# Kernel optimization log

Measured on AMD Instinct MI355X. Metric: run time of the kernel, lower is better.

The kernel has to match this reference:

```python
import jax, jax.numpy as jnp
import numpy as np

T, H, E, I, K = 8192, 2048, 32, 1024, 2


def setup_inputs() -> dict:
    key = jax.random.key(0)
    ks = jax.random.split(key, 6)
    s = 1.0 / np.sqrt(H)
    return {
        "hidden_states": jax.random.normal(ks[0], (T, H), dtype=jnp.float32),
        "router_logits": jax.random.normal(ks[1], (T, E), dtype=jnp.float32),
        "per_expert_scale": jax.random.uniform(ks[2], (E,), dtype=jnp.float32, minval=0.5, maxval=1.5),
        "w_gate": jax.random.normal(ks[3], (E, H, I), dtype=jnp.float32) * s,
        "w_up": jax.random.normal(ks[4], (E, H, I), dtype=jnp.float32) * s,
        "w_down": jax.random.normal(ks[5], (E, I, H), dtype=jnp.float32) * (1.0 / np.sqrt(I)),
        "top_k": K,
    }


def reference(hidden_states, router_logits, per_expert_scale, w_gate, w_up, w_down, top_k):
    num_tokens, hidden_dim = hidden_states.shape
    num_experts = w_gate.shape[0]
    # Gemma4 routing: top-k over raw logits, softmax over the k logits
    # (== full softmax renormalized over top-k), scaled per expert.
    topk_logits, topk_ids = jax.lax.top_k(router_logits, top_k)  # [T,K]
    topk_weights = jax.nn.softmax(topk_logits, axis=-1) * per_expert_scale[topk_ids]
    # Dense combine matrix [T,E]: weight for expert e if selected, else 0.
    cw = jnp.zeros((num_tokens, num_experts), hidden_states.dtype)
    cw = cw.at[jnp.arange(num_tokens)[:, None], topk_ids].add(
        topk_weights.astype(hidden_states.dtype))
    # Gated GELU MLP per expert, weighted accumulate (scan keeps memory small).
    def body(acc, ws):
        wg, wu, wd, c = ws  # c: [T] combine weight for this expert
        h = jax.nn.gelu(hidden_states @ wg, approximate=False) * (hidden_states @ wu)
        return acc + c[:, None] * (h @ wd), None
    acc0 = jnp.zeros_like(hidden_states)
    out, _ = jax.lax.scan(body, acc0, (w_gate, w_up, w_down, cw.T))
    return out
```

## Files before the change

kernel.cpp:

```cpp
#include <hip/hip_runtime.h>

#define T_TOK 8192
#define HDIM  2048
#define NEXP  32
#define IDIM  1024

#define BM 128
#define BN 128
#define BK 64
#define CAP (T_TOK*2 + NEXP*BM)
#define MAX_RT (CAP/BM)

typedef __attribute__((ext_vector_type(8))) short bh8;
typedef __attribute__((ext_vector_type(4))) float f4;

__device__ __forceinline__ unsigned short f2bf(float f) {
    unsigned u = __builtin_bit_cast(unsigned, f);
    u += 0x7FFFu + ((u >> 16) & 1u);
    return (unsigned short)(u >> 16);
}

__device__ __forceinline__ int swz(int row, int kb) {
    return row * 128 + (kb ^ ((row & 7) << 4));
}


__device__ __forceinline__ void top2(const float* __restrict__ l,
                                     int& b1, float& v1, int& b2, float& v2) {
    v1 = -1e30f; b1 = 0;
#pragma unroll
    for (int e = 0; e < NEXP; ++e) { float v = l[e]; if (v > v1) { v1 = v; b1 = e; } }
    v2 = -1e30f; b2 = 0;
#pragma unroll
    for (int e = 0; e < NEXP; ++e) { if (e == b1) continue; float v = l[e]; if (v > v2) { v2 = v; b2 = e; } }
}

__global__ void route_count_kernel(const float* __restrict__ logits, int* __restrict__ counts) {
    int t = blockIdx.x * blockDim.x + threadIdx.x;
    if (t >= T_TOK) return;
    int b1, b2; float v1, v2;
    top2(logits + (size_t)t * NEXP, b1, v1, b2, v2);
    atomicAdd(&counts[b1], 1);
    atomicAdd(&counts[b2], 1);
}

__global__ void offsets_kernel(const int* __restrict__ counts, int* __restrict__ offs) {
    if (threadIdx.x == 0) {
        int o = 0;
        for (int e = 0; e < NEXP; ++e) { offs[e] = o; o += (counts[e] + BM - 1) & ~(BM - 1); }
        offs[NEXP] = o;
    }
}

__global__ void route_scatter_kernel(const float* __restrict__ logits,
                                     const float* __restrict__ scale,
                                     const int* __restrict__ offs,
                                     int* __restrict__ cursor,
                                     int* __restrict__ row_tok,
                                     float* __restrict__ row_w) {
    int t = blockIdx.x * blockDim.x + threadIdx.x;
    if (t >= T_TOK) return;
    int b1, b2; float v1, v2;
    top2(logits + (size_t)t * NEXP, b1, v1, b2, v2);
    float e2 = expf(v2 - v1);
    float inv = 1.0f / (1.0f + e2);
    float w1 = scale[b1] * inv;
    float w2 = scale[b2] * e2 * inv;
    int p1 = offs[b1] + atomicAdd(&cursor[b1], 1);
    row_tok[p1] = t; row_w[p1] = w1;
    int p2 = offs[b2] + atomicAdd(&cursor[b2], 1);
    row_tok[p2] = t; row_w[p2] = w2;
}


__device__ __forceinline__ void stage_w(char* dst, const float* __restrict__ src,
                                        long stride, int wn, int wk) {
    float t[32];
#pragma unroll
    for (int kk = 0; kk < 32; ++kk) t[kk] = src[kk * stride];
#pragma unroll
    for (int j = 0; j < 4; ++j) {
        bh8 p;
#pragma unroll
        for (int i = 0; i < 8; ++i) p[i] = (short)f2bf(t[j * 8 + i]);
        *(bh8*)(dst + swz(wn, wk * 64 + j * 16)) = p;
    }
}


__launch_bounds__(256, 2)
__global__ void gemm1_kernel(const float* __restrict__ hs,
                             const float* __restrict__ wg,
                             const float* __restrict__ wu,
                             const int* __restrict__ offs,
                             const int* __restrict__ row_tok,
                             unsigned short* __restrict__ act) {
    __shared__ char lds[48 * 1024];
    char* Xb = lds;
    char* Gb = lds + 16384;
    char* Ub = lds + 32768;

    int rt = blockIdx.x >> 3;
    int nt = blockIdx.x & 7;
    int total = offs[NEXP];
    if (rt * BM >= total) return;
    int e = 0;
    while (offs[e + 1] <= rt * BM) e++;

    int tid = threadIdx.x;
    int lane = tid & 63;
    int wv = tid >> 6;
    int m0 = wv * 32;

    int sr = tid >> 1;
    int sh = tid & 1;
    int tok = row_tok[rt * BM + sr];
    const float* xsrc = hs + (size_t)(tok < 0 ? 0 : tok) * HDIM + sh * 32;

    int wn = tid & 127;
    int wk = tid >> 7;
    const float* wgs = wg + (size_t)e * HDIM * IDIM + (size_t)(wk * 32) * IDIM + nt * BN + wn;
    const float* wus = wu + (size_t)e * HDIM * IDIM + (size_t)(wk * 32) * IDIM + nt * BN + wn;

    f4 accG[2][8], accU[2][8];
#pragma unroll
    for (int m = 0; m < 2; ++m)
#pragma unroll
        for (int n = 0; n < 8; ++n) { accG[m][n] = (f4)0.0f; accU[m][n] = (f4)0.0f; }

    for (int kt = 0; kt < HDIM / BK; ++kt) {
        {
            float4 v[8];
#pragma unroll
            for (int j = 0; j < 8; ++j) v[j] = make_float4(0.f, 0.f, 0.f, 0.f);
            if (tok >= 0) {
                const float4* p = (const float4*)(xsrc + kt * BK);
#pragma unroll
                for (int j = 0; j < 8; ++j) v[j] = p[j];
            }
#pragma unroll
            for (int j = 0; j < 4; ++j) {
                float4 a = v[2 * j], b = v[2 * j + 1];
                bh8 p;
                p[0] = (short)f2bf(a.x); p[1] = (short)f2bf(a.y);
                p[2] = (short)f2bf(a.z); p[3] = (short)f2bf(a.w);
                p[4] = (short)f2bf(b.x); p[5] = (short)f2bf(b.y);
                p[6] = (short)f2bf(b.z); p[7] = (short)f2bf(b.w);
                *(bh8*)(Xb + swz(sr, sh * 64 + j * 16)) = p;
            }
        }
        stage_w(Gb, wgs + (size_t)kt * BK * IDIM, IDIM, wn, wk);
        stage_w(Ub, wus + (size_t)kt * BK * IDIM, IDIM, wn, wk);
        __syncthreads();

#pragma unroll
        for (int ks = 0; ks < 2; ++ks) {
            int kb = ks * 64 + ((lane >> 4) << 4);
            bh8 a0 = *(const bh8*)(Xb + swz(m0 + (lane & 15), kb));
            bh8 a1 = *(const bh8*)(Xb + swz(m0 + 16 + (lane & 15), kb));
#pragma unroll
            for (int n = 0; n < 8; ++n) {
                int nr = n * 16 + (lane & 15);
                bh8 bg = *(const bh8*)(Gb + swz(nr, kb));
                bh8 bu = *(const bh8*)(Ub + swz(nr, kb));
                accG[0][n] = __builtin_amdgcn_mfma_f32_16x16x32_bf16(a0, bg, accG[0][n], 0, 0, 0);
                accG[1][n] = __builtin_amdgcn_mfma_f32_16x16x32_bf16(a1, bg, accG[1][n], 0, 0, 0);
                accU[0][n] = __builtin_amdgcn_mfma_f32_16x16x32_bf16(a0, bu, accU[0][n], 0, 0, 0);
                accU[1][n] = __builtin_amdgcn_mfma_f32_16x16x32_bf16(a1, bu, accU[1][n], 0, 0, 0);
            }
        }
        __syncthreads();
    }

    int col0 = nt * BN + (lane & 15);
#pragma unroll
    for (int m = 0; m < 2; ++m) {
        int rbase = rt * BM + m0 + m * 16 + ((lane >> 4) << 2);
#pragma unroll
        for (int n = 0; n < 8; ++n) {
#pragma unroll
            for (int i = 0; i < 4; ++i) {
                float g = accG[m][n][i], u = accU[m][n][i];
                float gl = 0.5f * g * (1.0f + erff(g * 0.70710678118654752f));
                act[(size_t)(rbase + i) * IDIM + col0 + n * 16] = f2bf(gl * u);
            }
        }
    }
}


__launch_bounds__(256, 2)
__global__ void gemm2_kernel(const unsigned short* __restrict__ act,
                             const float* __restrict__ wd,
                             const int* __restrict__ offs,
                             const int* __restrict__ row_tok,
                             const float* __restrict__ row_w,
                             float* __restrict__ out) {
    __shared__ char lds[32 * 1024];
    char* Xb = lds;
    char* Db = lds + 16384;

    int rt = blockIdx.x >> 4;
    int nt = blockIdx.x & 15;
    int total = offs[NEXP];
    if (rt * BM >= total) return;
    int e = 0;
    while (offs[e + 1] <= rt * BM) e++;

    int tid = threadIdx.x;
    int lane = tid & 63;
    int wv = tid >> 6;
    int m0 = wv * 32;

    int sr = tid >> 1;
    int sh = tid & 1;
    const unsigned short* asrc = act + (size_t)(rt * BM + sr) * IDIM + sh * 32;

    int wn = tid & 127;
    int wk = tid >> 7;
    const float* wds = wd + (size_t)e * IDIM * HDIM + (size_t)(wk * 32) * HDIM + nt * BN + wn;

    f4 acc[2][8];
#pragma unroll
    for (int m = 0; m < 2; ++m)
#pragma unroll
        for (int n = 0; n < 8; ++n) acc[m][n] = (f4)0.0f;

    for (int kt = 0; kt < IDIM / BK; ++kt) {
        {
            const bh8* p = (const bh8*)(asrc + kt * BK);
#pragma unroll
            for (int j = 0; j < 4; ++j)
                *(bh8*)(Xb + swz(sr, sh * 64 + j * 16)) = p[j];
        }
        stage_w(Db, wds + (size_t)kt * BK * HDIM, HDIM, wn, wk);
        __syncthreads();

#pragma unroll
        for (int ks = 0; ks < 2; ++ks) {
            int kb = ks * 64 + ((lane >> 4) << 4);
            bh8 a0 = *(const bh8*)(Xb + swz(m0 + (lane & 15), kb));
            bh8 a1 = *(const bh8*)(Xb + swz(m0 + 16 + (lane & 15), kb));
#pragma unroll
            for (int n = 0; n < 8; ++n) {
                int nr = n * 16 + (lane & 15);
                bh8 b = *(const bh8*)(Db + swz(nr, kb));
                acc[0][n] = __builtin_amdgcn_mfma_f32_16x16x32_bf16(a0, b, acc[0][n], 0, 0, 0);
                acc[1][n] = __builtin_amdgcn_mfma_f32_16x16x32_bf16(a1, b, acc[1][n], 0, 0, 0);
            }
        }
        __syncthreads();
    }

    int col0 = nt * BN + (lane & 15);
#pragma unroll
    for (int m = 0; m < 2; ++m) {
        int rbase = rt * BM + m0 + m * 16 + ((lane >> 4) << 2);
#pragma unroll
        for (int i = 0; i < 4; ++i) {
            int r = rbase + i;
            int tok = row_tok[r];
            if (tok < 0) continue;
            float w = row_w[r];
            float* op = out + (size_t)tok * HDIM + col0;
#pragma unroll
            for (int n = 0; n < 8; ++n)
                atomicAdd(op + n * 16, acc[m][n][i] * w);
        }
    }
}


extern "C" void kernel_launch(void* const* d_in, const int* in_sizes, int n_in,
                              void* d_out, int out_size, void* d_ws, size_t ws_size,
                              hipStream_t stream) {
    const float* hs     = (const float*)d_in[0];
    const float* logits = (const float*)d_in[1];
    const float* scale  = (const float*)d_in[2];
    const float* wg     = (const float*)d_in[3];
    const float* wu     = (const float*)d_in[4];
    const float* wd     = (const float*)d_in[5];
    float* out = (float*)d_out;

    char* ws = (char*)d_ws;
    int*   counts  = (int*)ws;
    int*   cursor  = counts + 32;
    int*   offs    = cursor + 32;
    int*   row_tok = (int*)(ws + 512);
    float* row_w   = (float*)(ws + 512 + (size_t)CAP * 4);
    unsigned short* act = (unsigned short*)(ws + 512 + (size_t)CAP * 8);

    hipMemsetAsync(counts, 0, 512, stream);
    hipMemsetAsync(row_tok, 0xFF, (size_t)CAP * 4, stream);
    hipMemsetAsync(out, 0, (size_t)out_size * sizeof(float), stream);

    route_count_kernel<<<T_TOK / 256, 256, 0, stream>>>(logits, counts);
    offsets_kernel<<<1, 64, 0, stream>>>(counts, offs);
    route_scatter_kernel<<<T_TOK / 256, 256, 0, stream>>>(logits, scale, offs, cursor, row_tok, row_w);
    gemm1_kernel<<<MAX_RT * 8, 256, 0, stream>>>(hs, wg, wu, offs, row_tok, act);
    gemm2_kernel<<<MAX_RT * 16, 256, 0, stream>>>(act, wd, offs, row_tok, row_w, out);
}
```

Measured before the change: 805.3 us.

## Pre-convert activations and weights to transposed bf16, use direct-to-LDS loads in GEMMs

New measurement: 745.9 us. 1.08x faster.

```diff
diff --git a/kernel.cpp b/kernel.cpp
--- a/kernel.cpp
+++ b/kernel.cpp
@@ -22,6 +22,13 @@
 
 __device__ __forceinline__ int swz(int row, int kb) {
     return row * 128 + (kb ^ ((row & 7) << 4));
+}
+
+__device__ __forceinline__ void gload16(const void* g, void* l) {
+    __builtin_amdgcn_global_load_lds(
+        (const __attribute__((address_space(1))) unsigned int*)g,
+        (__attribute__((address_space(3))) unsigned int*)l,
+        16, 0, 0);
 }
 
 
@@ -73,6 +80,244 @@
 }
 
 
+__global__ void cvt_hs_kernel(const float* __restrict__ in, unsigned short* __restrict__ out) {
+    size_t i = ((size_t)blockIdx.x * 256 + threadIdx.x) * 8;
+    float4 a = *(const float4*)(in + i);
+    float4 b = *(const float4*)(in + i + 4);
+    bh8 v;
+    v[0] = (short)f2bf(a.x); v[1] = (short)f2bf(a.y);
+    v[2] = (short)f2bf(a.z); v[3] = (short)f2bf(a.w);
+    v[4] = (short)f2bf(b.x); v[5] = (short)f2bf(b.y);
+    v[6] = (short)f2bf(b.z); v[7] = (short)f2bf(b.w);
+    *(bh8*)(out + i) = v;
+}
+
+__global__ void transpose_cvt_kernel(const float* __restrict__ in,
+                                     unsigned short* __restrict__ out,
+                                     int K, int N, int tilesN) {
+    int bid = blockIdx.x;
+    int e = bid >> 9;
+    int tile = bid & 511;
+    int k0 = (tile / tilesN) * 64;
+    int n0 = (tile % tilesN) * 64;
+    const float* src = in + (size_t)e * K * N;
+    unsigned short* dst = out + (size_t)e * K * N;
+    int tid = threadIdx.x, l = tid & 63, w = tid >> 6;
+    int n = n0 + w * 16 + (l >> 2);
+#pragma unroll
+    for (int p = 0; p < 2; ++p) {
+        int kc = k0 + p * 32 + (l & 3) * 8;
+        const float* s = src + (size_t)kc * N + n;
+        bh8 v;
+#pragma unroll
+        for (int j = 0; j < 8; ++j) v[j] = (short)f2bf(s[(size_t)j * N]);
+        *(bh8*)(dst + (size_t)n * K + kc) = v;
+    }
+}
+
+__launch_bounds__(256, 2)
+__global__ void gemm1n_kernel(const unsigned short* __restrict__ hsb,
+                              const unsigned short* __restrict__ wgT,
+                              const unsigned short* __restrict__ wuT,
+                              const int* __restrict__ offs,
+                              const int* __restrict__ row_tok,
+                              unsigned short* __restrict__ act) {
+    __shared__ char lds[49152];
+    char* Xb = lds;
+    char* Gb = lds + 16384;
+    char* Ub = lds + 32768;
+
+    int rt = blockIdx.x >> 3;
+    int nt = blockIdx.x & 7;
+    int total = offs[NEXP];
+    if (rt * BM >= total) return;
+    int e = 0;
+    while (offs[e + 1] <= rt * BM) e++;
+
+    int tid = threadIdx.x, l = tid & 63, wv = tid >> 6;
+    int wm = wv >> 1, wn = wv & 1;
+
+    unsigned srcChunk = ((l & 7) * 16) ^ ((l >> 3) << 4);
+
+    unsigned xoff[4], goff[4], uoff[4];
+#pragma unroll
+    for (int i = 0; i < 4; ++i) {
+        int r = i * 32 + wv * 8 + (l >> 3);
+        int tok = row_tok[rt * BM + r];
+        if (tok < 0) tok = 0;
+        xoff[i] = (unsigned)tok * (HDIM * 2) + srcChunk;
+        unsigned wrow = (unsigned)e * IDIM + nt * BN + r;
+        goff[i] = wrow * (HDIM * 2) + srcChunk;
+        uoff[i] = goff[i];
+    }
+
+    f4 accG[4][4], accU[4][4];
+#pragma unroll
+    for (int mi = 0; mi < 4; ++mi)
+#pragma unroll
+        for (int ni = 0; ni < 4; ++ni) { accG[mi][ni] = (f4)0.0f; accU[mi][ni] = (f4)0.0f; }
+
+    const char* hsc = (const char*)hsb;
+    const char* wgc = (const char*)wgT;
+    const char* wuc = (const char*)wuT;
+
+    for (int kt = 0; kt < HDIM / BK; ++kt) {
+        unsigned kby = kt * 128;
+#pragma unroll
+        for (int i = 0; i < 4; ++i) {
+            char* dX = Xb + i * 4096 + wv * 1024;
+            gload16(hsc + (size_t)xoff[i] + kby, dX);
+        }
+#pragma unroll
+        for (int i = 0; i < 4; ++i) {
+            char* dG = Gb + i * 4096 + wv * 1024;
+            gload16(wgc + (size_t)goff[i] + kby, dG);
+        }
+#pragma unroll
+        for (int i = 0; i < 4; ++i) {
+            char* dU = Ub + i * 4096 + wv * 1024;
+            gload16(wuc + (size_t)uoff[i] + kby, dU);
+        }
+        __syncthreads();
+
+#pragma unroll
+        for (int ks = 0; ks < 2; ++ks) {
+            int kb = ks * 64 + ((l >> 4) << 4);
+            bh8 a[4], g[4], u[4];
+#pragma unroll
+            for (int mi = 0; mi < 4; ++mi)
+                a[mi] = *(const bh8*)(Xb + swz(wm * 64 + mi * 16 + (l & 15), kb));
+#pragma unroll
+            for (int ni = 0; ni < 4; ++ni) {
+                int nr = wn * 64 + ni * 16 + (l & 15);
+                g[ni] = *(const bh8*)(Gb + swz(nr, kb));
+                u[ni] = *(const bh8*)(Ub + swz(nr, kb));
+            }
+#pragma unroll
+            for (int mi = 0; mi < 4; ++mi)
+#pragma unroll
+                for (int ni = 0; ni < 4; ++ni) {
+                    accG[mi][ni] = __builtin_amdgcn_mfma_f32_16x16x32_bf16(a[mi], g[ni], accG[mi][ni], 0, 0, 0);
+                    accU[mi][ni] = __builtin_amdgcn_mfma_f32_16x16x32_bf16(a[mi], u[ni], accU[mi][ni], 0, 0, 0);
+                }
+        }
+        __syncthreads();
+    }
+
+    char* actc = (char*)act;
+#pragma unroll
+    for (int mi = 0; mi < 4; ++mi) {
+#pragma unroll
+        for (int i = 0; i < 4; ++i) {
+            int r = rt * BM + wm * 64 + mi * 16 + ((l >> 4) << 2) + i;
+            size_t rowbase = (size_t)r * (IDIM * 2);
+            int rs = (r & 7) << 4;
+#pragma unroll
+            for (int ni = 0; ni < 4; ++ni) {
+                int col = nt * BN + wn * 64 + ni * 16 + (l & 15);
+                float gv = accG[mi][ni][i], uv = accU[mi][ni][i];
+                float gl = 0.5f * gv * (1.0f + erff(gv * 0.70710678118654752f));
+                *(unsigned short*)(actc + rowbase + ((col * 2) ^ rs)) = f2bf(gl * uv);
+            }
+        }
+    }
+}
+
+__launch_bounds__(256, 2)
+__global__ void gemm2n_kernel(const unsigned short* __restrict__ act,
+                              const unsigned short* __restrict__ wdT,
+                              const int* __restrict__ offs,
+                              const int* __restrict__ row_tok,
+                              const float* __restrict__ row_w,
+                              float* __restrict__ out) {
+    __shared__ char lds[49152];
+    char* Xb = lds;
+    char* Db = lds + 16384;
+
+    int rt = blockIdx.x >> 3;
+    int nt = blockIdx.x & 7;
+    int total = offs[NEXP];
+    if (rt * BM >= total) return;
+    int e = 0;
+    while (offs[e + 1] <= rt * BM) e++;
+
+    int tid = threadIdx.x, l = tid & 63, wv = tid >> 6;
+    int wm = wv >> 1, wn = wv & 1;
+
+    unsigned srcChunk = ((l & 7) * 16) ^ ((l >> 3) << 4);
+
+    unsigned aoff[4];
+#pragma unroll
+    for (int i = 0; i < 4; ++i) {
+        int r = i * 32 + wv * 8 + (l >> 3);
+        aoff[i] = (unsigned)(rt * BM + r) * (IDIM * 2) + (l & 7) * 16;
+    }
+    unsigned doff[8];
+#pragma unroll
+    for (int i = 0; i < 8; ++i) {
+        int r = i * 32 + wv * 8 + (l >> 3);
+        doff[i] = ((unsigned)e * HDIM + nt * 256 + r) * (IDIM * 2) + srcChunk;
+    }
+
+    f4 acc[4][8];
+#pragma unroll
+    for (int mi = 0; mi < 4; ++mi)
+#pragma unroll
+        for (int ni = 0; ni < 8; ++ni) acc[mi][ni] = (f4)0.0f;
+
+    const char* actc = (const char*)act;
+    const char* wdc = (const char*)wdT;
+
+    for (int kt = 0; kt < IDIM / BK; ++kt) {
+        unsigned kby = kt * 128;
+#pragma unroll
+        for (int i = 0; i < 4; ++i) {
+            char* dX = Xb + i * 4096 + wv * 1024;
+            gload16(actc + (size_t)aoff[i] + kby, dX);
+        }
+#pragma unroll
+        for (int i = 0; i < 8; ++i) {
+            char* dD = Db + i * 4096 + wv * 1024;
+            gload16(wdc + (size_t)doff[i] + kby, dD);
+        }
+        __syncthreads();
+
+#pragma unroll
+        for (int ks = 0; ks < 2; ++ks) {
+            int kb = ks * 64 + ((l >> 4) << 4);
+            bh8 a[4], b[8];
+#pragma unroll
+            for (int mi = 0; mi < 4; ++mi)
+                a[mi] = *(const bh8*)(Xb + swz(wm * 64 + mi * 16 + (l & 15), kb));
+#pragma unroll
+            for (int ni = 0; ni < 8; ++ni)
+                b[ni] = *(const bh8*)(Db + swz(wn * 128 + ni * 16 + (l & 15), kb));
+#pragma unroll
+            for (int mi = 0; mi < 4; ++mi)
+#pragma unroll
+                for (int ni = 0; ni < 8; ++ni)
+                    acc[mi][ni] = __builtin_amdgcn_mfma_f32_16x16x32_bf16(a[mi], b[ni], acc[mi][ni], 0, 0, 0);
+        }
+        __syncthreads();
+    }
+
+#pragma unroll
+    for (int mi = 0; mi < 4; ++mi) {
+#pragma unroll
+        for (int i = 0; i < 4; ++i) {
+            int r = rt * BM + wm * 64 + mi * 16 + ((l >> 4) << 2) + i;
+            int tok = row_tok[r];
+            if (tok < 0) continue;
+            float w = row_w[r];
+            float* op = out + (size_t)tok * HDIM + nt * 256 + wn * 128 + (l & 15);
+#pragma unroll
+            for (int ni = 0; ni < 8; ++ni)
+                atomicAdd(op + ni * 16, acc[mi][ni][i] * w);
+        }
+    }
+}
+
+
 __device__ __forceinline__ void stage_w(char* dst, const float* __restrict__ src,
                                         long stride, int wn, int wk) {
     float t[32];
@@ -86,7 +331,6 @@
         *(bh8*)(dst + swz(wn, wk * 64 + j * 16)) = p;
     }
 }
-
 
 __launch_bounds__(256, 2)
 __global__ void gemm1_kernel(const float* __restrict__ hs,
@@ -188,7 +432,6 @@
     }
 }
 
-
 __launch_bounds__(256, 2)
 __global__ void gemm2_kernel(const unsigned short* __restrict__ act,
                              const float* __restrict__ wd,
@@ -290,6 +533,12 @@
     float* row_w   = (float*)(ws + 512 + (size_t)CAP * 4);
     unsigned short* act = (unsigned short*)(ws + 512 + (size_t)CAP * 8);
 
+    size_t actB  = (size_t)CAP * IDIM * 2;
+    size_t hsB   = (size_t)T_TOK * HDIM * 2;
+    size_t wTB   = (size_t)NEXP * IDIM * HDIM * 2;
+    size_t baseA = 512 + (size_t)CAP * 8;
+    size_t needA = baseA + actB + hsB + 2 * wTB;
+
     hipMemsetAsync(counts, 0, 512, stream);
     hipMemsetAsync(row_tok, 0xFF, (size_t)CAP * 4, stream);
     hipMemsetAsync(out, 0, (size_t)out_size * sizeof(float), stream);
@@ -297,6 +546,21 @@
     route_count_kernel<<<T_TOK / 256, 256, 0, stream>>>(logits, counts);
     offsets_kernel<<<1, 64, 0, stream>>>(counts, offs);
     route_scatter_kernel<<<T_TOK / 256, 256, 0, stream>>>(logits, scale, offs, cursor, row_tok, row_w);
-    gemm1_kernel<<<MAX_RT * 8, 256, 0, stream>>>(hs, wg, wu, offs, row_tok, act);
-    gemm2_kernel<<<MAX_RT * 16, 256, 0, stream>>>(act, wd, offs, row_tok, row_w, out);
-}
+
+    if (ws_size >= needA) {
+        unsigned short* hsb = (unsigned short*)(ws + baseA + actB);
+        unsigned short* wgT = (unsigned short*)(ws + baseA + actB + hsB);
+        unsigned short* wuT = (unsigned short*)(ws + baseA + actB + hsB + wTB);
+        unsigned short* wdT = wgT;
+
+        cvt_hs_kernel<<<(T_TOK * HDIM) / (256 * 8), 256, 0, stream>>>(hs, hsb);
+        transpose_cvt_kernel<<<NEXP * 512, 256, 0, stream>>>(wg, wgT, HDIM, IDIM, 16);
+        transpose_cvt_kernel<<<NEXP * 512, 256, 0, stream>>>(wu, wuT, HDIM, IDIM, 16);
+        gemm1n_kernel<<<MAX_RT * 8, 256, 0, stream>>>(hsb, wgT, wuT, offs, row_tok, act);
+        transpose_cvt_kernel<<<NEXP * 512, 256, 0, stream>>>(wd, wdT, IDIM, HDIM, 32);
+        gemm2n_kernel<<<MAX_RT * 8, 256, 0, stream>>>(act, wdT, offs, row_tok, row_w, out);
+    } else {
+        gemm1_kernel<<<MAX_RT * 8, 256, 0, stream>>>(hs, wg, wu, offs, row_tok, act);
+        gemm2_kernel<<<MAX_RT * 16, 256, 0, stream>>>(act, wd, offs, row_tok, row_w, out);
+    }
+}
```

## Pre-convert activations to bf16 and software-pipeline both expert GEMMs with async LDS loads

Applied to the files above, without the earlier changes.

Result: slower. 2.120 ms (+163.2%).

```diff
diff --git a/kernel.cpp b/kernel.cpp
--- a/kernel.cpp
+++ b/kernel.cpp
@@ -22,6 +22,16 @@
 
 __device__ __forceinline__ int swz(int row, int kb) {
     return row * 128 + (kb ^ ((row & 7) << 4));
+}
+__device__ __forceinline__ int swzW(int row, int kb) {
+    return row * 128 + (kb ^ (((row >> 2) & 7) << 4));
+}
+
+__device__ __forceinline__ void gload16(const void* g, void* l) {
+    __builtin_amdgcn_global_load_lds(
+        (const __attribute__((address_space(1))) unsigned int*)g,
+        (__attribute__((address_space(3))) unsigned int*)l,
+        16, 0, 0);
 }
 
 
@@ -72,33 +82,30 @@
     row_tok[p2] = t; row_w[p2] = w2;
 }
 
-
-__device__ __forceinline__ void stage_w(char* dst, const float* __restrict__ src,
-                                        long stride, int wn, int wk) {
-    float t[32];
-#pragma unroll
-    for (int kk = 0; kk < 32; ++kk) t[kk] = src[kk * stride];
-#pragma unroll
-    for (int j = 0; j < 4; ++j) {
-        bh8 p;
-#pragma unroll
-        for (int i = 0; i < 8; ++i) p[i] = (short)f2bf(t[j * 8 + i]);
-        *(bh8*)(dst + swz(wn, wk * 64 + j * 16)) = p;
-    }
-}
-
+__global__ void cvt_hs_kernel(const float* __restrict__ in, unsigned short* __restrict__ out) {
+    size_t i = ((size_t)blockIdx.x * 256 + threadIdx.x) * 8;
+    float4 a = *(const float4*)(in + i);
+    float4 b = *(const float4*)(in + i + 4);
+    bh8 v;
+    v[0] = (short)f2bf(a.x); v[1] = (short)f2bf(a.y);
+    v[2] = (short)f2bf(a.z); v[3] = (short)f2bf(a.w);
+    v[4] = (short)f2bf(b.x); v[5] = (short)f2bf(b.y);
+    v[6] = (short)f2bf(b.z); v[7] = (short)f2bf(b.w);
+    *(bh8*)(out + i) = v;
+}
 
 __launch_bounds__(256, 2)
-__global__ void gemm1_kernel(const float* __restrict__ hs,
-                             const float* __restrict__ wg,
-                             const float* __restrict__ wu,
-                             const int* __restrict__ offs,
-                             const int* __restrict__ row_tok,
-                             unsigned short* __restrict__ act) {
-    __shared__ char lds[48 * 1024];
-    char* Xb = lds;
-    char* Gb = lds + 16384;
-    char* Ub = lds + 32768;
+__global__ void gemm1f_kernel(const unsigned short* __restrict__ hsb,
+                              const float* __restrict__ wg,
+                              const float* __restrict__ wu,
+                              const int* __restrict__ offs,
+                              const int* __restrict__ row_tok,
+                              unsigned short* __restrict__ act) {
+    __shared__ char lds[65536];
+    char* Xb0 = lds;
+    char* Xb1 = lds + 16384;
+    char* Gb  = lds + 32768;
+    char* Ub  = lds + 49152;
 
     int rt = blockIdx.x >> 3;
     int nt = blockIdx.x & 7;
@@ -107,98 +114,134 @@
     int e = 0;
     while (offs[e + 1] <= rt * BM) e++;
 
-    int tid = threadIdx.x;
-    int lane = tid & 63;
-    int wv = tid >> 6;
-    int m0 = wv * 32;
-
-    int sr = tid >> 1;
-    int sh = tid & 1;
-    int tok = row_tok[rt * BM + sr];
-    const float* xsrc = hs + (size_t)(tok < 0 ? 0 : tok) * HDIM + sh * 32;
-
-    int wn = tid & 127;
-    int wk = tid >> 7;
-    const float* wgs = wg + (size_t)e * HDIM * IDIM + (size_t)(wk * 32) * IDIM + nt * BN + wn;
-    const float* wus = wu + (size_t)e * HDIM * IDIM + (size_t)(wk * 32) * IDIM + nt * BN + wn;
-
-    f4 accG[2][8], accU[2][8];
-#pragma unroll
-    for (int m = 0; m < 2; ++m)
-#pragma unroll
-        for (int n = 0; n < 8; ++n) { accG[m][n] = (f4)0.0f; accU[m][n] = (f4)0.0f; }
+    int tid = threadIdx.x, l = tid & 63, wv = tid >> 6;
+    int wm = wv >> 1, wn = wv & 1;
+
+    unsigned srcChunk = ((l & 7) * 16) ^ ((l >> 3) << 4);
+    unsigned xoff[4];
+#pragma unroll
+    for (int i = 0; i < 4; ++i) {
+        int r = i * 32 + wv * 8 + (l >> 3);
+        int tok = row_tok[rt * BM + r];
+        if (tok < 0) tok = 0;
+        xoff[i] = (unsigned)tok * (HDIM * 2) + srcChunk;
+    }
+    const char* hsc = (const char*)hsb;
+
+    int g32 = tid & 31, kc8 = tid >> 5;
+    const float* wgp = wg + (size_t)e * HDIM * IDIM + (size_t)kc8 * 8 * IDIM + nt * BN + g32 * 4;
+    const float* wup = wu + (size_t)e * HDIM * IDIM + (size_t)kc8 * 8 * IDIM + nt * BN + g32 * 4;
+    float4 wGr[8], wUr[8];
+
+    f4 accG[4][4], accU[4][4];
+#pragma unroll
+    for (int mi = 0; mi < 4; ++mi)
+#pragma unroll
+        for (int ni = 0; ni < 4; ++ni) { accG[mi][ni] = (f4)0.0f; accU[mi][ni] = (f4)0.0f; }
+
+#define LOADW1(KT) {                                                        \
+    size_t kb_ = (size_t)(KT) * 64;                                         \
+    _Pragma("unroll")                                                       \
+    for (int j = 0; j < 8; ++j) {                                           \
+        wGr[j] = *(const float4*)(wgp + (kb_ + j) * IDIM);                  \
+        wUr[j] = *(const float4*)(wup + (kb_ + j) * IDIM);                  \
+    } }
+
+#define WRITEW1() {                                                         \
+    _Pragma("unroll")                                                       \
+    for (int c = 0; c < 4; ++c) {                                           \
+        int n_ = g32 * 4 + c;                                               \
+        int wb_ = n_ * 128 + ((kc8 * 16) ^ ((g32 & 7) << 4));               \
+        bh8 pg, pu;                                                         \
+        _Pragma("unroll")                                                   \
+        for (int j = 0; j < 8; ++j) {                                       \
+            float gg = (c == 0) ? wGr[j].x : (c == 1) ? wGr[j].y : (c == 2) ? wGr[j].z : wGr[j].w; \
+            float uu = (c == 0) ? wUr[j].x : (c == 1) ? wUr[j].y : (c == 2) ? wUr[j].z : wUr[j].w; \
+            pg[j] = (short)f2bf(gg);                                        \
+            pu[j] = (short)f2bf(uu);                                        \
+        }                                                                   \
+        *(bh8*)(Gb + wb_) = pg;                                             \
+        *(bh8*)(Ub + wb_) = pu;                                             \
+    } }
+
+#define LOADX1(KT, XB) {                                                    \
+    unsigned kby_ = (unsigned)(KT) * 128;                                   \
+    _Pragma("unroll")                                                       \
+    for (int i = 0; i < 4; ++i)                                             \
+        gload16(hsc + (size_t)xoff[i] + kby_, (XB) + i * 4096 + wv * 1024); \
+    }
+
+    LOADW1(0);
+    LOADX1(0, Xb0);
+    WRITEW1();
+    __syncthreads();
 
     for (int kt = 0; kt < HDIM / BK; ++kt) {
-        {
-            float4 v[8];
-#pragma unroll
-            for (int j = 0; j < 8; ++j) v[j] = make_float4(0.f, 0.f, 0.f, 0.f);
-            if (tok >= 0) {
-                const float4* p = (const float4*)(xsrc + kt * BK);
-#pragma unroll
-                for (int j = 0; j < 8; ++j) v[j] = p[j];
+        char* cur = (kt & 1) ? Xb1 : Xb0;
+        char* nxt = (kt & 1) ? Xb0 : Xb1;
+        if (kt < HDIM / BK - 1) {
+            LOADW1(kt + 1);
+            LOADX1(kt + 1, nxt);
+        }
+#pragma unroll
+        for (int ks = 0; ks < 2; ++ks) {
+            int kb = ks * 64 + ((l >> 4) << 4);
+            bh8 a[4], g[4], u[4];
+#pragma unroll
+            for (int mi = 0; mi < 4; ++mi)
+                a[mi] = *(const bh8*)(cur + swz(wm * 64 + mi * 16 + (l & 15), kb));
+#pragma unroll
+            for (int ni = 0; ni < 4; ++ni) {
+                int nr = wn * 64 + ni * 16 + (l & 15);
+                g[ni] = *(const bh8*)(Gb + swzW(nr, kb));
+                u[ni] = *(const bh8*)(Ub + swzW(nr, kb));
             }
 #pragma unroll
-            for (int j = 0; j < 4; ++j) {
-                float4 a = v[2 * j], b = v[2 * j + 1];
-                bh8 p;
-                p[0] = (short)f2bf(a.x); p[1] = (short)f2bf(a.y);
-                p[2] = (short)f2bf(a.z); p[3] = (short)f2bf(a.w);
-                p[4] = (short)f2bf(b.x); p[5] = (short)f2bf(b.y);
-                p[6] = (short)f2bf(b.z); p[7] = (short)f2bf(b.w);
-                *(bh8*)(Xb + swz(sr, sh * 64 + j * 16)) = p;
+            for (int mi = 0; mi < 4; ++mi)
+#pragma unroll
+                for (int ni = 0; ni < 4; ++ni) {
+                    accG[mi][ni] = __builtin_amdgcn_mfma_f32_16x16x32_bf16(a[mi], g[ni], accG[mi][ni], 0, 0, 0);
+                    accU[mi][ni] = __builtin_amdgcn_mfma_f32_16x16x32_bf16(a[mi], u[ni], accU[mi][ni], 0, 0, 0);
+                }
+        }
+        __syncthreads();
+        if (kt < HDIM / BK - 1) WRITEW1();
+        __syncthreads();
+    }
+
+    char* actc = (char*)act;
+#pragma unroll
+    for (int mi = 0; mi < 4; ++mi) {
+#pragma unroll
+        for (int i = 0; i < 4; ++i) {
+            int r = rt * BM + wm * 64 + mi * 16 + ((l >> 4) << 2) + i;
+            size_t rowbase = (size_t)r * (IDIM * 2);
+            int rs = (r & 7) << 4;
+#pragma unroll
+            for (int ni = 0; ni < 4; ++ni) {
+                int col = nt * BN + wn * 64 + ni * 16 + (l & 15);
+                float gv = accG[mi][ni][i], uv = accU[mi][ni][i];
+                float gl = 0.5f * gv * (1.0f + erff(gv * 0.70710678118654752f));
+                *(unsigned short*)(actc + rowbase + ((col * 2) ^ rs)) = f2bf(gl * uv);
             }
         }
-        stage_w(Gb, wgs + (size_t)kt * BK * IDIM, IDIM, wn, wk);
-        stage_w(Ub, wus + (size_t)kt * BK * IDIM, IDIM, wn, wk);
-        __syncthreads();
-
-#pragma unroll
-        for (int ks = 0; ks < 2; ++ks) {
-            int kb = ks * 64 + ((lane >> 4) << 4);
-            bh8 a0 = *(const bh8*)(Xb + swz(m0 + (lane & 15), kb));
-            bh8 a1 = *(const bh8*)(Xb + swz(m0 + 16 + (lane & 15), kb));
-#pragma unroll
-            for (int n = 0; n < 8; ++n) {
-                int nr = n * 16 + (lane & 15);
-                bh8 bg = *(const bh8*)(Gb + swz(nr, kb));
-                bh8 bu = *(const bh8*)(Ub + swz(nr, kb));
-                accG[0][n] = __builtin_amdgcn_mfma_f32_16x16x32_bf16(a0, bg, accG[0][n], 0, 0, 0);
-                accG[1][n] = __builtin_amdgcn_mfma_f32_16x16x32_bf16(a1, bg, accG[1][n], 0, 0, 0);
-                accU[0][n] = __builtin_amdgcn_mfma_f32_16x16x32_bf16(a0, bu, accU[0][n], 0, 0, 0);
-                accU[1][n] = __builtin_amdgcn_mfma_f32_16x16x32_bf16(a1, bu, accU[1][n], 0, 0, 0);
-            }
-        }
-        __syncthreads();
-    }
-
-    int col0 = nt * BN + (lane & 15);
-#pragma unroll
-    for (int m = 0; m < 2; ++m) {
-        int rbase = rt * BM + m0 + m * 16 + ((lane >> 4) << 2);
-#pragma unroll
-        for (int n = 0; n < 8; ++n) {
-#pragma unroll
-            for (int i = 0; i < 4; ++i) {
-                float g = accG[m][n][i], u = accU[m][n][i];
-                float gl = 0.5f * g * (1.0f + erff(g * 0.70710678118654752f));
-                act[(size_t)(rbase + i) * IDIM + col0 + n * 16] = f2bf(gl * u);
-            }
-        }
-    }
-}
-
-
-__launch_bounds__(256, 2)
-__global__ void gemm2_kernel(const unsigned short* __restrict__ act,
-                             const float* __restrict__ wd,
-                             const int* __restrict__ offs,
-                             const int* __restrict__ row_tok,
-                             const float* __restrict__ row_w,
-                             float* __restrict__ out) {
-    __shared__ char lds[32 * 1024];
-    char* Xb = lds;
-    char* Db = lds + 16384;
+    }
+#undef LOADW1
+#undef WRITEW1
+#undef LOADX1
+}
+
+__launch_bounds__(256, 3)
+__global__ void gemm2f_kernel(const unsigned short* __restrict__ act,
+                              const float* __restrict__ wd,
+                              const int* __restrict__ offs,
+                              const int* __restrict__ row_tok,
+                              const float* __restrict__ row_w,
+                              float* __restrict__ out) {
+    __shared__ char lds[49152];
+    char* Xb0 = lds;
+    char* Xb1 = lds + 16384;
+    char* Db  = lds + 32768;
 
     int rt = blockIdx.x >> 4;
     int nt = blockIdx.x & 15;
@@ -207,67 +250,105 @@
     int e = 0;
     while (offs[e + 1] <= rt * BM) e++;
 
-    int tid = threadIdx.x;
-    int lane = tid & 63;
-    int wv = tid >> 6;
-    int m0 = wv * 32;
-
-    int sr = tid >> 1;
-    int sh = tid & 1;
-    const unsigned short* asrc = act + (size_t)(rt * BM + sr) * IDIM + sh * 32;
-
-    int wn = tid & 127;
-    int wk = tid >> 7;
-    const float* wds = wd + (size_t)e * IDIM * HDIM + (size_t)(wk * 32) * HDIM + nt * BN + wn;
-
-    f4 acc[2][8];
-#pragma unroll
-    for (int m = 0; m < 2; ++m)
-#pragma unroll
-        for (int n = 0; n < 8; ++n) acc[m][n] = (f4)0.0f;
+    int tid = threadIdx.x, l = tid & 63, wv = tid >> 6;
+    int wm = wv >> 1, wn = wv & 1;
+
+    unsigned aoff[4];
+#pragma unroll
+    for (int i = 0; i < 4; ++i) {
+        int r = i * 32 + wv * 8 + (l >> 3);
+        aoff[i] = (unsigned)(rt * BM + r) * (IDIM * 2) + (l & 7) * 16;
+    }
+    const char* actc = (const char*)act;
+
+    int g32 = tid & 31, kc8 = tid >> 5;
+    const float* wdp = wd + (size_t)e * IDIM * HDIM + (size_t)kc8 * 8 * HDIM + nt * BN + g32 * 4;
+    float4 wDr[8];
+
+    f4 acc[4][4];
+#pragma unroll
+    for (int mi = 0; mi < 4; ++mi)
+#pragma unroll
+        for (int ni = 0; ni < 4; ++ni) acc[mi][ni] = (f4)0.0f;
+
+#define LOADW2(KT) {                                                        \
+    size_t kb_ = (size_t)(KT) * 64;                                         \
+    _Pragma("unroll")                                                       \
+    for (int j = 0; j < 8; ++j)                                             \
+        wDr[j] = *(const float4*)(wdp + (kb_ + j) * HDIM);                  \
+    }
+
+#define WRITEW2() {                                                         \
+    _Pragma("unroll")                                                       \
+    for (int c = 0; c < 4; ++c) {                                           \
+        int n_ = g32 * 4 + c;                                               \
+        int wb_ = n_ * 128 + ((kc8 * 16) ^ ((g32 & 7) << 4));               \
+        bh8 pd;                                                             \
+        _Pragma("unroll")                                                   \
+        for (int j = 0; j < 8; ++j) {                                       \
+            float dd = (c == 0) ? wDr[j].x : (c == 1) ? wDr[j].y : (c == 2) ? wDr[j].z : wDr[j].w; \
+            pd[j] = (short)f2bf(dd);                                        \
+        }                                                                   \
+        *(bh8*)(Db + wb_) = pd;                                             \
+    } }
+
+#define LOADX2(KT, XB) {                                                    \
+    unsigned kby_ = (unsigned)(KT) * 128;                                   \
+    _Pragma("unroll")                                                       \
+    for (int i = 0; i < 4; ++i)                                             \
+        gload16(actc + (size_t)aoff[i] + kby_, (XB) + i * 4096 + wv * 1024);\
+    }
+
+    LOADW2(0);
+    LOADX2(0, Xb0);
+    WRITEW2();
+    __syncthreads();
 
     for (int kt = 0; kt < IDIM / BK; ++kt) {
-        {
-            const bh8* p = (const bh8*)(asrc + kt * BK);
-#pragma unroll
-            for (int j = 0; j < 4; ++j)
-                *(bh8*)(Xb + swz(sr, sh * 64 + j * 16)) = p[j];
-        }
-        stage_w(Db, wds + (size_t)kt * BK * HDIM, HDIM, wn, wk);
+        char* cur = (kt & 1) ? Xb1 : Xb0;
+        char* nxt = (kt & 1) ? Xb0 : Xb1;
+        if (kt < IDIM / BK - 1) {
+            LOADW2(kt + 1);
+            LOADX2(kt + 1, nxt);
+        }
+#pragma unroll
+        for (int ks = 0; ks < 2; ++ks) {
+            int kb = ks * 64 + ((l >> 4) << 4);
+            bh8 a[4], b[4];
+#pragma unroll
+            for (int mi = 0; mi < 4; ++mi)
+                a[mi] = *(const bh8*)(cur + swz(wm * 64 + mi * 16 + (l & 15), kb));
+#pragma unroll
+            for (int ni = 0; ni < 4; ++ni)
+                b[ni] = *(const bh8*)(Db + swzW(wn * 64 + ni * 16 + (l & 15), kb));
+#pragma unroll
+            for (int mi = 0; mi < 4; ++mi)
+#pragma unroll
+                for (int ni = 0; ni < 4; ++ni)
+                    acc[mi][ni] = __builtin_amdgcn_mfma_f32_16x16x32_bf16(a[mi], b[ni], acc[mi][ni], 0, 0, 0);
+        }
         __syncthreads();
-
-#pragma unroll
-        for (int ks = 0; ks < 2; ++ks) {
-            int kb = ks * 64 + ((lane >> 4) << 4);
-            bh8 a0 = *(const bh8*)(Xb + swz(m0 + (lane & 15), kb));
-            bh8 a1 = *(const bh8*)(Xb + swz(m0 + 16 + (lane & 15), kb));
-#pragma unroll
-            for (int n = 0; n < 8; ++n) {
-                int nr = n * 16 + (lane & 15);
-                bh8 b = *(const bh8*)(Db + swz(nr, kb));
-                acc[0][n] = __builtin_amdgcn_mfma_f32_16x16x32_bf16(a0, b, acc[0][n], 0, 0, 0);
-                acc[1][n] = __builtin_amdgcn_mfma_f32_16x16x32_bf16(a1, b, acc[1][n], 0, 0, 0);
-            }
-        }
+        if (kt < IDIM / BK - 1) WRITEW2();
         __syncthreads();
     }
 
-    int col0 = nt * BN + (lane & 15);
-#pragma unroll
-    for (int m = 0; m < 2; ++m) {
-        int rbase = rt * BM + m0 + m * 16 + ((lane >> 4) << 2);
+#pragma unroll
+    for (int mi = 0; mi < 4; ++mi) {
 #pragma unroll
         for (int i = 0; i < 4; ++i) {
-            int r = rbase + i;
+            int r = rt * BM + wm * 64 + mi * 16 + ((l >> 4) << 2) + i;
             int tok = row_tok[r];
             if (tok < 0) continue;
             float w = row_w[r];
-            float* op = out + (size_t)tok * HDIM + col0;
-#pragma unroll
-            for (int n = 0; n < 8; ++n)
-                atomicAdd(op + n * 16, acc[m][n][i] * w);
-        }
-    }
+            float* op = out + (size_t)tok * HDIM + nt * BN + wn * 64 + (l & 15);
+#pragma unroll
+            for (int ni = 0; ni < 4; ++ni)
+                atomicAdd(op + ni * 16, acc[mi][ni][i] * w);
+        }
+    }
+#undef LOADW2
+#undef WRITEW2
+#undef LOADX2
 }
 
 
@@ -289,6 +370,8 @@
     int*   row_tok = (int*)(ws + 512);
     float* row_w   = (float*)(ws + 512 + (size_t)CAP * 4);
     unsigned short* act = (unsigned short*)(ws + 512 + (size_t)CAP * 8);
+    size_t actB = (size_t)CAP * IDIM * 2;
+    unsigned short* hsb = (unsigned short*)(ws + 512 + (size_t)CAP * 8 + actB);
 
     hipMemsetAsync(counts, 0, 512, stream);
     hipMemsetAsync(row_tok, 0xFF, (size_t)CAP * 4, stream);
@@ -297,6 +380,7 @@
     route_count_kernel<<<T_TOK / 256, 256, 0, stream>>>(logits, counts);
     offsets_kernel<<<1, 64, 0, stream>>>(counts, offs);
     route_scatter_kernel<<<T_TOK / 256, 256, 0, stream>>>(logits, scale, offs, cursor, row_tok, row_w);
-    gemm1_kernel<<<MAX_RT * 8, 256, 0, stream>>>(hs, wg, wu, offs, row_tok, act);
-    gemm2_kernel<<<MAX_RT * 16, 256, 0, stream>>>(act, wd, offs, row_tok, row_w, out);
-}
+    cvt_hs_kernel<<<(T_TOK * HDIM) / (256 * 8), 256, 0, stream>>>(hs, hsb);
+    gemm1f_kernel<<<MAX_RT * 8, 256, 0, stream>>>(hsb, wg, wu, offs, row_tok, act);
+    gemm2f_kernel<<<MAX_RT * 16, 256, 0, stream>>>(act, wd, offs, row_tok, row_w, out);
+}
```
